# Optimization experiments

Measured on AMD Instinct MI355X. Metric: run time of the kernel, lower is better.

Reference implementation:

```python
import jax, jax.numpy as jnp
import numpy as np

B_SZ, N_INST, D_IN, D_OUT, C_COMP, M_RANK = 512, 4, 1024, 1024, 64, 256

def setup_inputs() -> dict:
    key = jax.random.key(0)
    k1, k2, k3, k4 = jax.random.split(key, 4)
    x = jax.random.normal(k1, (B_SZ, N_INST, D_IN), dtype=jnp.float32)
    A = jax.random.normal(k2, (N_INST, C_COMP, D_IN, M_RANK), dtype=jnp.float32) * 0.02
    Bp = jax.random.normal(k3, (N_INST, C_COMP, M_RANK, D_OUT), dtype=jnp.float32) * 0.02
    topk_mask = jax.random.randint(k4, (B_SZ, N_INST, C_COMP), 0, 2, dtype=jnp.int32)
    return {"x": x, "A": A, "B": Bp, "topk_mask": topk_mask}

def reference(x, A, B, topk_mask):
    # inner: [b, i, C, m]
    inner = jnp.einsum('bid,icdm->bicm', x, A)
    inner = inner * topk_mask.astype(inner.dtype)[..., None]
    # comp: [b, i, C, d_out]
    comp = jnp.einsum('bicm,icmo->bico', inner, B)
    # sum over components C -> [b, i, d_out]
    return comp.sum(axis=2)
```

## Files before the change

### kernel.cpp

```cpp
#include <hip/hip_runtime.h>
#include <hip/hip_bf16.h>
#include <stdint.h>

#define B_SZ   512
#define NINST  4
#define D_IN   1024
#define D_OUTD 1024
#define CCOMP  64
#define MRANK  256
#define KTOT   (CCOMP*MRANK)

typedef __attribute__((ext_vector_type(4))) float  f32x4;
typedef __attribute__((ext_vector_type(8))) __bf16 bf16x8;
typedef __attribute__((ext_vector_type(4))) __bf16 bf16x4;

__device__ inline void gload16(const void* g, void* l) {
  __builtin_amdgcn_global_load_lds(
      (const __attribute__((address_space(1))) void*)g,
      (__attribute__((address_space(3))) void*)l, 16, 0, 0);
}

#define BARN(N) do { \
  asm volatile("s_waitcnt lgkmcnt(0) vmcnt(" #N ")" ::: "memory"); \
  __builtin_amdgcn_sched_barrier(0); \
  __builtin_amdgcn_s_barrier(); \
  __builtin_amdgcn_sched_barrier(0); } while (0)

__global__ __launch_bounds__(256)
void xcvt_kernel(const float* __restrict__ x, __bf16* __restrict__ xbf)
{
  const int total = (B_SZ*NINST*D_IN) / 4;
  for (int v = blockIdx.x*256 + threadIdx.x; v < total; v += gridDim.x*256) {
    const int k4 = v & 255;
    const int i  = (v >> 8) & 3;
    const int b  = v >> 10;
    f32x4 f = ((const f32x4*)x)[v];
    bf16x4 h; h[0]=(__bf16)f.x; h[1]=(__bf16)f.y; h[2]=(__bf16)f.z; h[3]=(__bf16)f.w;
    ((bf16x4*)xbf)[((size_t)i*B_SZ + b)*256 + k4] = h;
  }
}

__global__ __launch_bounds__(512, 1)
void p1_kernel(const __bf16* __restrict__ xbf, const float* __restrict__ A,
               const int* __restrict__ mask, __bf16* __restrict__ inner)
{
  const int bid = blockIdx.x;
  const int L   = (bid & 7) * 64 + (bid >> 3);
  const int bt  = L & 1;
  const int ic  = L >> 1;
  const int i   = ic >> 6;
  const int c   = ic & 63;
  const int b0  = bt * 256;
  const int NSTEP = 16;

  const int tid  = threadIdx.x;
  const int lane = tid & 63;
  const int wid  = tid >> 6;
  const int wr   = wid >> 2;
  const int wc   = wid & 3;

  __shared__ __align__(16) char smem[163840];
  __bf16* Xs = (__bf16*)smem;
  __bf16* As = (__bf16*)(smem + 98304);

  f32x4 acc[8][4];
#pragma unroll
  for (int a_ = 0; a_ < 8; ++a_)
#pragma unroll
    for (int b_ = 0; b_ < 4; ++b_)
      acc[a_][b_] = (f32x4){0.f, 0.f, 0.f, 0.f};

  const __bf16* xbase = xbf + ((size_t)i * B_SZ + b0) * D_IN;
  const float*  Abase = A + (size_t)ic * D_IN * MRANK;

  const int bo = tid & 255;
  const int bg = tid >> 8;
  float areg[4][8];

  auto stageX = [&](int slot, int kt) {
#pragma unroll
    for (int q = 0; q < 4; ++q) {
      const int u   = wid*4 + q;
      const int row = u*8 + (lane >> 3);
      const int kch = (lane & 7) ^ (row & 7);
      gload16(xbase + (size_t)row * D_IN + kt*64 + kch*8,
              Xs + slot*16384 + u*512);
    }
  };
  auto loadA = [&](int kt) {
#pragma unroll
    for (int q = 0; q < 4; ++q)
#pragma unroll
      for (int j = 0; j < 8; ++j)
        areg[q][j] = Abase[(size_t)(kt*64 + (bg*4+q)*8 + j)*MRANK + bo];
  };
  auto writeA = [&](int buf) {
#pragma unroll
    for (int q = 0; q < 4; ++q) {
      const int oct = bg*4 + q;
      bf16x8 h;
#pragma unroll
      for (int j = 0; j < 8; ++j) h[j] = (__bf16)areg[q][j];
      *(bf16x8*)(As + buf*16384 + bo*64 + ((oct ^ (bo & 7)))*8) = h;
    }
  };

  loadA(0);
  stageX(0, 0);
  stageX(1, 1);
  writeA(0);
  BARN(4);

#pragma unroll 1
  for (int t = 0; t < NSTEP; ++t) {
    const int slot = t % 3;
    const int buf  = t & 1;
    if (t+1 < NSTEP) loadA(t+1);
    if (t+2 < NSTEP) stageX((t+2) % 3, t+2);
#pragma unroll
    for (int kk = 0; kk < 2; ++kk) {
      const int oct = kk*4 + (lane >> 4);
      bf16x8 bf[4];
#pragma unroll
      for (int ni = 0; ni < 4; ++ni) {
        const int col = wc*64 + ni*16 + (lane & 15);
        bf[ni] = *(const bf16x8*)(As + buf*16384 + col*64 + ((oct ^ (col & 7)))*8);
      }
#pragma unroll
      for (int mh = 0; mh < 2; ++mh) {
        bf16x8 af[4];
#pragma unroll
        for (int mi = 0; mi < 4; ++mi) {
          const int row = wr*128 + (mh*4 + mi)*16 + (lane & 15);
          af[mi] = *(const bf16x8*)(Xs + slot*16384 + row*64 + ((oct ^ (row & 7)))*8);
        }
        __builtin_amdgcn_s_setprio(1);
#pragma unroll
        for (int ni = 0; ni < 4; ++ni)
#pragma unroll
          for (int mi = 0; mi < 4; ++mi)
            acc[mh*4+mi][ni] = __builtin_amdgcn_mfma_f32_16x16x32_bf16(
                af[mi], bf[ni], acc[mh*4+mi][ni], 0, 0, 0);
        __builtin_amdgcn_s_setprio(0);
      }
    }
    if (t+1 < NSTEP) writeA(buf ^ 1);
    if (t >= NSTEP-2) BARN(0); else BARN(4);
  }

  __bf16* obase = inner + ((size_t)i * B_SZ + b0) * KTOT + (size_t)c * MRANK;
#pragma unroll
  for (int mi = 0; mi < 8; ++mi) {
    float mv[4];
#pragma unroll
    for (int j = 0; j < 4; ++j) {
      const int row = wr*128 + mi*16 + (lane >> 4)*4 + j;
      mv[j] = (float)mask[(size_t)(b0 + row) * (NINST*CCOMP) + i*CCOMP + c];
    }
#pragma unroll
    for (int ni = 0; ni < 4; ++ni) {
      const int colL = wc*64 + ni*16 + (lane & 15);
#pragma unroll
      for (int j = 0; j < 4; ++j) {
        const int rowL = wr*128 + mi*16 + (lane >> 4)*4 + j;
        obase[(size_t)rowL * KTOT + colL] = (__bf16)(acc[mi][ni][j] * mv[j]);
      }
    }
  }
}

__global__ __launch_bounds__(512, 1)
void p2_kernel(const __bf16* __restrict__ inner, const float* __restrict__ Bm,
               float* __restrict__ dst, int nks)
{
  const int bid = blockIdx.x;
  const int nwg = gridDim.x;
  const int L   = (bid & 7) * (nwg >> 3) + (bid >> 3);
  const int tile = L & 7;
  const int rest = L >> 3;
  const int ks  = rest % nks;
  const int i   = rest / nks;
  const int mt  = tile & 1;
  const int nt  = tile >> 1;
  const int b0  = mt * 256;
  const int o0  = nt * 256;
  const int NSTEP = (KTOT/64) / nks;
  const int kb0   = ks * NSTEP;

  const int tid  = threadIdx.x;
  const int lane = tid & 63;
  const int wid  = tid >> 6;
  const int wr   = wid >> 2;
  const int wc   = wid & 3;

  __shared__ __align__(16) char smem[163840];
  __bf16* As = (__bf16*)smem;
  __bf16* Bs = (__bf16*)(smem + 98304);

  f32x4 acc[8][4];
#pragma unroll
  for (int a_ = 0; a_ < 8; ++a_)
#pragma unroll
    for (int b_ = 0; b_ < 4; ++b_)
      acc[a_][b_] = (f32x4){0.f, 0.f, 0.f, 0.f};

  const __bf16* ibase = inner + ((size_t)i * B_SZ + b0) * KTOT;
  const float*  Bbase = Bm + (size_t)i * KTOT * D_OUTD + o0;

  const int bo = tid & 255;
  const int bg = tid >> 8;
  float breg[4][8];

  auto stageA = [&](int slot, int kt) {
#pragma unroll
    for (int q = 0; q < 4; ++q) {
      const int u   = wid*4 + q;
      const int row = u*8 + (lane >> 3);
      const int kch = (lane & 7) ^ (row & 7);
      gload16(ibase + (size_t)row * KTOT + (size_t)(kb0 + kt)*64 + kch*8,
              As + slot*16384 + u*512);
    }
  };
  auto loadB = [&](int kt) {
#pragma unroll
    for (int q = 0; q < 4; ++q)
#pragma unroll
      for (int j = 0; j < 8; ++j)
        breg[q][j] = Bbase[(size_t)((size_t)(kb0 + kt)*64 + (bg*4+q)*8 + j)*D_OUTD + bo];
  };
  auto writeB = [&](int buf) {
#pragma unroll
    for (int q = 0; q < 4; ++q) {
      const int oct = bg*4 + q;
      bf16x8 h;
#pragma unroll
      for (int j = 0; j < 8; ++j) h[j] = (__bf16)breg[q][j];
      *(bf16x8*)(Bs + buf*16384 + bo*64 + ((oct ^ (bo & 7)))*8) = h;
    }
  };

  loadB(0);
  stageA(0, 0);
  stageA(1, 1);
  writeB(0);
  BARN(4);

#pragma unroll 1
  for (int t = 0; t < NSTEP; ++t) {
    const int aslot = t % 3;
    const int bbuf  = t & 1;
    if (t+1 < NSTEP) loadB(t+1);
    if (t+2 < NSTEP) stageA((t+2) % 3, t+2);
#pragma unroll
    for (int kk = 0; kk < 2; ++kk) {
      const int oct = kk*4 + (lane >> 4);
      bf16x8 bf[4];
#pragma unroll
      for (int ni = 0; ni < 4; ++ni) {
        const int col = wc*64 + ni*16 + (lane & 15);
        bf[ni] = *(const bf16x8*)(Bs + bbuf*16384 + col*64 + ((oct ^ (col & 7)))*8);
      }
#pragma unroll
      for (int mh = 0; mh < 2; ++mh) {
        bf16x8 af[4];
#pragma unroll
        for (int mi = 0; mi < 4; ++mi) {
          const int row = wr*128 + (mh*4 + mi)*16 + (lane & 15);
          af[mi] = *(const bf16x8*)(As + aslot*16384 + row*64 + ((oct ^ (row & 7)))*8);
        }
        __builtin_amdgcn_s_setprio(1);
#pragma unroll
        for (int ni = 0; ni < 4; ++ni)
#pragma unroll
          for (int mi = 0; mi < 4; ++mi)
            acc[mh*4+mi][ni] = __builtin_amdgcn_mfma_f32_16x16x32_bf16(
                af[mi], bf[ni], acc[mh*4+mi][ni], 0, 0, 0);
        __builtin_amdgcn_s_setprio(0);
      }
    }
    if (t+1 < NSTEP) writeB(bbuf ^ 1);
    if (t >= NSTEP-2) BARN(0); else BARN(4);
  }

  float* obase = dst + (size_t)ks * ((size_t)B_SZ*NINST*D_OUTD)
               + ((size_t)b0 * NINST + i) * D_OUTD + o0;
#pragma unroll
  for (int mi = 0; mi < 8; ++mi)
#pragma unroll
    for (int ni = 0; ni < 4; ++ni) {
      const int colL = wc*64 + ni*16 + (lane & 15);
#pragma unroll
      for (int j = 0; j < 4; ++j) {
        const int rowL = wr*128 + mi*16 + (lane >> 4)*4 + j;
        obase[(size_t)rowL * (NINST*D_OUTD) + colL] = acc[mi][ni][j];
      }
    }
}

__global__ __launch_bounds__(256)
void reduce_kernel(const float* __restrict__ part, float* __restrict__ out, int nks)
{
  const int total = (B_SZ*NINST*D_OUTD) / 4;
  for (int v = blockIdx.x*256 + threadIdx.x; v < total; v += gridDim.x*256) {
    f32x4 s = ((const f32x4*)part)[v];
    for (int ks = 1; ks < nks; ++ks)
      s += ((const f32x4*)part)[(size_t)ks*total + v];
    ((f32x4*)out)[v] = s;
  }
}

extern "C" void kernel_launch(void* const* d_in, const int* in_sizes, int n_in,
                              void* d_out, int out_size, void* d_ws, size_t ws_size,
                              hipStream_t stream) {
  const float* x    = (const float*)d_in[0];
  const float* A    = (const float*)d_in[1];
  const float* Bm   = (const float*)d_in[2];
  const int*   mask = (const int*)d_in[3];

  const size_t innerB = (size_t)NINST * B_SZ * KTOT * 2;
  const size_t xbfB   = (size_t)NINST * B_SZ * D_IN * 2;
  const size_t partB  = (size_t)B_SZ * NINST * D_OUTD * 4;

  char* p = (char*)d_ws;
  __bf16* inner = (__bf16*)p;             p += innerB;
  __bf16* xbf   = (__bf16*)p;             p += xbfB;
  const size_t used = (size_t)(p - (char*)d_ws);

  int nks = 1;
  if      (ws_size >= used + 8*partB) nks = 8;
  else if (ws_size >= used + 4*partB) nks = 4;
  else if (ws_size >= used + 2*partB) nks = 2;
  float* part = (nks > 1) ? (float*)p : (float*)d_out;

  xcvt_kernel<<<dim3(1024),  dim3(256), 0, stream>>>(x, xbf);
  p1_kernel<<<dim3(512),     dim3(512), 0, stream>>>(xbf, A, mask, inner);
  p2_kernel<<<dim3(32*nks),  dim3(512), 0, stream>>>(inner, Bm, part, nks);
  if (nks > 1)
    reduce_kernel<<<dim3(1024), dim3(256), 0, stream>>>(part, (float*)d_out, nks);
}
```

Measured before the change: 223.8 us.

## Halve p1 tile width along rank and prefetch A two steps ahead

The first-stage GEMM now splits each (instance, component) rank dimension into two 128-wide halves, which doubles the grid to 1024 workgroups and halves the accumulator and A-tile footprint per workgroup. A loads are issued two k-steps ahead into alternating register sets, and the wait count is relaxed so more global loads stay in flight. The aim is better occupancy and CU coverage and more latency hiding for the fp32 A reads. In exchange, each X tile is now loaded twice, once per rank half, and each workgroup has less MFMA work per byte of LDS traffic.

```diff
diff --git a/kernel.cpp b/kernel.cpp
--- a/kernel.cpp
+++ b/kernel.cpp
@@ -45,37 +45,39 @@
                const int* __restrict__ mask, __bf16* __restrict__ inner)
 {
   const int bid = blockIdx.x;
-  const int L   = (bid & 7) * 64 + (bid >> 3);
+  const int L   = (bid & 7) * 128 + (bid >> 3);
   const int bt  = L & 1;
-  const int ic  = L >> 1;
+  const int mt  = (L >> 1) & 1;
+  const int ic  = L >> 2;
   const int i   = ic >> 6;
   const int c   = ic & 63;
   const int b0  = bt * 256;
+  const int m0  = mt * 128;
   const int NSTEP = 16;
 
   const int tid  = threadIdx.x;
   const int lane = tid & 63;
   const int wid  = tid >> 6;
-  const int wr   = wid >> 2;
-  const int wc   = wid & 3;
-
-  __shared__ __align__(16) char smem[163840];
+  const int wr   = wid >> 1;
+  const int wc   = wid & 1;
+
+  __shared__ __align__(16) char smem[131072];
   __bf16* Xs = (__bf16*)smem;
   __bf16* As = (__bf16*)(smem + 98304);
 
-  f32x4 acc[8][4];
-#pragma unroll
-  for (int a_ = 0; a_ < 8; ++a_)
+  f32x4 acc[4][4];
+#pragma unroll
+  for (int a_ = 0; a_ < 4; ++a_)
 #pragma unroll
     for (int b_ = 0; b_ < 4; ++b_)
       acc[a_][b_] = (f32x4){0.f, 0.f, 0.f, 0.f};
 
   const __bf16* xbase = xbf + ((size_t)i * B_SZ + b0) * D_IN;
-  const float*  Abase = A + (size_t)ic * D_IN * MRANK;
-
-  const int bo = tid & 255;
-  const int bg = tid >> 8;
-  float areg[4][8];
+  const float*  Abase = A + (size_t)ic * D_IN * MRANK + m0;
+
+  const int bo = tid & 127;
+  const int bg = tid >> 7;
+  float a0[2][8], a1[2][8];
 
   auto stageX = [&](int slot, int kt) {
 #pragma unroll
@@ -87,36 +89,38 @@
               Xs + slot*16384 + u*512);
     }
   };
-  auto loadA = [&](int kt) {
-#pragma unroll
-    for (int q = 0; q < 4; ++q)
+  auto loadA = [&](int kt, float (&ar)[2][8]) {
+#pragma unroll
+    for (int q = 0; q < 2; ++q)
 #pragma unroll
       for (int j = 0; j < 8; ++j)
-        areg[q][j] = Abase[(size_t)(kt*64 + (bg*4+q)*8 + j)*MRANK + bo];
-  };
-  auto writeA = [&](int buf) {
-#pragma unroll
-    for (int q = 0; q < 4; ++q) {
-      const int oct = bg*4 + q;
+        ar[q][j] = Abase[(size_t)(kt*64 + (bg*2+q)*8 + j)*MRANK + bo];
+  };
+  auto writeA = [&](int buf, const float (&ar)[2][8]) {
+#pragma unroll
+    for (int q = 0; q < 2; ++q) {
+      const int oct = bg*2 + q;
       bf16x8 h;
 #pragma unroll
-      for (int j = 0; j < 8; ++j) h[j] = (__bf16)areg[q][j];
-      *(bf16x8*)(As + buf*16384 + bo*64 + ((oct ^ (bo & 7)))*8) = h;
-    }
-  };
-
-  loadA(0);
+      for (int j = 0; j < 8; ++j) h[j] = (__bf16)ar[q][j];
+      *(bf16x8*)(As + buf*8192 + bo*64 + ((oct ^ (bo & 7)))*8) = h;
+    }
+  };
+
   stageX(0, 0);
+  loadA(0, a0); loadA(1, a1);
   stageX(1, 1);
-  writeA(0);
-  BARN(4);
+  writeA(0, a0);
+  BARN(20);
 
 #pragma unroll 1
   for (int t = 0; t < NSTEP; ++t) {
     const int slot = t % 3;
     const int buf  = t & 1;
-    if (t+1 < NSTEP) loadA(t+1);
-    if (t+2 < NSTEP) stageX((t+2) % 3, t+2);
+    if (t+2 < NSTEP) {
+      if (!(t & 1)) loadA(t+2, a0); else loadA(t+2, a1);
+      stageX((t+2) % 3, t+2);
+    }
 #pragma unroll
     for (int kk = 0; kk < 2; ++kk) {
       const int oct = kk*4 + (lane >> 4);
@@ -124,37 +128,36 @@
 #pragma unroll
       for (int ni = 0; ni < 4; ++ni) {
         const int col = wc*64 + ni*16 + (lane & 15);
-        bf[ni] = *(const bf16x8*)(As + buf*16384 + col*64 + ((oct ^ (col & 7)))*8);
-      }
-#pragma unroll
-      for (int mh = 0; mh < 2; ++mh) {
-        bf16x8 af[4];
-#pragma unroll
-        for (int mi = 0; mi < 4; ++mi) {
-          const int row = wr*128 + (mh*4 + mi)*16 + (lane & 15);
-          af[mi] = *(const bf16x8*)(Xs + slot*16384 + row*64 + ((oct ^ (row & 7)))*8);
-        }
-        __builtin_amdgcn_s_setprio(1);
-#pragma unroll
-        for (int ni = 0; ni < 4; ++ni)
-#pragma unroll
-          for (int mi = 0; mi < 4; ++mi)
-            acc[mh*4+mi][ni] = __builtin_amdgcn_mfma_f32_16x16x32_bf16(
-                af[mi], bf[ni], acc[mh*4+mi][ni], 0, 0, 0);
-        __builtin_amdgcn_s_setprio(0);
-      }
-    }
-    if (t+1 < NSTEP) writeA(buf ^ 1);
-    if (t >= NSTEP-2) BARN(0); else BARN(4);
-  }
-
-  __bf16* obase = inner + ((size_t)i * B_SZ + b0) * KTOT + (size_t)c * MRANK;
-#pragma unroll
-  for (int mi = 0; mi < 8; ++mi) {
+        bf[ni] = *(const bf16x8*)(As + buf*8192 + col*64 + ((oct ^ (col & 7)))*8);
+      }
+      bf16x8 af[4];
+#pragma unroll
+      for (int mi = 0; mi < 4; ++mi) {
+        const int row = wr*64 + mi*16 + (lane & 15);
+        af[mi] = *(const bf16x8*)(Xs + slot*16384 + row*64 + ((oct ^ (row & 7)))*8);
+      }
+      __builtin_amdgcn_s_setprio(1);
+#pragma unroll
+      for (int ni = 0; ni < 4; ++ni)
+#pragma unroll
+        for (int mi = 0; mi < 4; ++mi)
+          acc[mi][ni] = __builtin_amdgcn_mfma_f32_16x16x32_bf16(
+              af[mi], bf[ni], acc[mi][ni], 0, 0, 0);
+      __builtin_amdgcn_s_setprio(0);
+    }
+    if (t+1 < NSTEP) {
+      if (!(t & 1)) writeA(buf ^ 1, a1); else writeA(buf ^ 1, a0);
+    }
+    if (t < NSTEP-2) BARN(20); else BARN(0);
+  }
+
+  __bf16* obase = inner + ((size_t)i * B_SZ + b0) * KTOT + (size_t)c * MRANK + m0;
+#pragma unroll
+  for (int mi = 0; mi < 4; ++mi) {
     float mv[4];
 #pragma unroll
     for (int j = 0; j < 4; ++j) {
-      const int row = wr*128 + mi*16 + (lane >> 4)*4 + j;
+      const int row = wr*64 + mi*16 + (lane >> 4)*4 + j;
       mv[j] = (float)mask[(size_t)(b0 + row) * (NINST*CCOMP) + i*CCOMP + c];
     }
 #pragma unroll
@@ -162,7 +165,7 @@
       const int colL = wc*64 + ni*16 + (lane & 15);
 #pragma unroll
       for (int j = 0; j < 4; ++j) {
-        const int rowL = wr*128 + mi*16 + (lane >> 4)*4 + j;
+        const int rowL = wr*64 + mi*16 + (lane >> 4)*4 + j;
         obase[(size_t)rowL * KTOT + colL] = (__bf16)(acc[mi][ni][j] * mv[j]);
       }
     }
@@ -333,7 +336,7 @@
   float* part = (nks > 1) ? (float*)p : (float*)d_out;
 
   xcvt_kernel<<<dim3(1024),  dim3(256), 0, stream>>>(x, xbf);
-  p1_kernel<<<dim3(512),     dim3(512), 0, stream>>>(xbf, A, mask, inner);
+  p1_kernel<<<dim3(1024),    dim3(512), 0, stream>>>(xbf, A, mask, inner);
   p2_kernel<<<dim3(32*nks),  dim3(512), 0, stream>>>(inner, Bm, part, nks);
   if (nks > 1)
     reduce_kernel<<<dim3(1024), dim3(256), 0, stream>>>(part, (float*)d_out, nks);
```

Result: slower. 263.6 us (+17.8%).
